# Optimization experiments

Hardware: AMD Instinct MI355X
Metric: run time of the kernel (lower is better)

Reference implementation:

```python
import jax, jax.numpy as jnp
import numpy as np
import math

EMB_DIM = 2048
HEAD_NUMS = 16
HEAD_DIM = EMB_DIM // HEAD_NUMS


def setup_inputs() -> dict:
    key = jax.random.key(0)
    k1, k2, k3, k4, k5 = jax.random.split(key, 5)
    B, S = 2, 2048
    X = jax.random.normal(k1, (B, S, EMB_DIM), dtype=jnp.float32)
    mask = jnp.ones((B, S), dtype=jnp.int32)
    # torch nn.Linear weights: [out_features, in_features]
    W_qkv = jax.random.normal(k2, (3 * EMB_DIM, EMB_DIM), dtype=jnp.float32) / math.sqrt(EMB_DIM)
    b_qkv = jax.random.normal(k3, (3 * EMB_DIM,), dtype=jnp.float32) * 0.01
    W_o = jax.random.normal(k4, (EMB_DIM, EMB_DIM), dtype=jnp.float32) / math.sqrt(EMB_DIM)
    b_o = jax.random.normal(k5, (EMB_DIM,), dtype=jnp.float32) * 0.01
    return {"X": X, "mask": mask, "W_qkv": W_qkv, "b_qkv": b_qkv, "W_o": W_o, "b_o": b_o}


def _rope_tables(seq_len):
    # Bug-faithful to source: exponent divides by full emb_dim, not head_dim.
    angle = 1.0 / jnp.power(10000.0, jnp.arange(0, HEAD_DIM, 2, dtype=jnp.float32) / EMB_DIM)
    t = jnp.arange(seq_len, dtype=jnp.float32)
    freqs = t[:, None] * angle[None, :]            # [S, HEAD_DIM//2]
    freqs = jnp.repeat(freqs, 2, axis=-1)          # [S, HEAD_DIM] (repeat_interleave)
    return jnp.cos(freqs), jnp.sin(freqs)


def _trans(x):
    # de-interleave pairs, then concat([-odd, even]) along last dim (as in source)
    B, H, S, D = x.shape
    xr = x.reshape(B, H, S, D // 2, 2)
    x1, x2 = xr[..., 0], xr[..., 1]
    return jnp.concatenate([-x2, x1], axis=-1)


def reference(X, mask, W_qkv, b_qkv, W_o, b_o):
    B, S, E = X.shape
    cos, sin = _rope_tables(S)                      # [S, HEAD_DIM]
    qkv = X @ W_qkv.T + b_qkv                       # [B, S, 3E]
    qkv = qkv.reshape(B, S, 3, HEAD_NUMS, HEAD_DIM).transpose(2, 0, 3, 1, 4)
    Q, K, V = qkv[0], qkv[1], qkv[2]                # [B, H, S, D]
    c = cos[None, None, :, :]
    s = sin[None, None, :, :]
    Q = c * Q + s * _trans(Q)
    K = c * K + s * _trans(K)
    scores = jnp.einsum('bhqd,bhkd->bhqk', Q, K) / math.sqrt(HEAD_DIM)
    pad = mask[:, None, None, :]                    # [B,1,1,S]
    scores = jnp.where(pad == 0, -1e9, scores)
    attn = jax.nn.softmax(scores, axis=-1)          # dropout = identity (eval)
    out = jnp.einsum('bhqk,bhkd->bhqd', attn, V)    # [B,H,S,D]
    out = out.transpose(0, 2, 1, 3).reshape(B, S, E)
    return out @ W_o.T + b_o
```

## Files before the change

### kernel.cpp

```cpp
#include <hip/hip_runtime.h>
#include <hip/hip_bf16.h>
#include <math.h>

typedef __bf16 bf16x8 __attribute__((ext_vector_type(8)));
typedef float  f32x4  __attribute__((ext_vector_type(4)));
typedef float  f32x16 __attribute__((ext_vector_type(16)));
typedef unsigned short ushort_t;
typedef ushort_t us4 __attribute__((ext_vector_type(4)));

#define MFMA16(a, b, c) __builtin_amdgcn_mfma_f32_16x16x32_bf16((a), (b), (c), 0, 0, 0)
#define MFMA32(a, b, c) __builtin_amdgcn_mfma_f32_32x32x16_bf16((a), (b), (c), 0, 0, 0)

__device__ __forceinline__ float bf2f(ushort_t h) {
    union { unsigned u; float f; } v; v.u = ((unsigned)h) << 16; return v.f;
}
__device__ __forceinline__ ushort_t f2bf(float x) {
    union { float f; unsigned u; } v; v.f = x;
    unsigned r = v.u + 0x7FFFu + ((v.u >> 16) & 1u);
    return (ushort_t)(r >> 16);
}
__device__ __forceinline__ void gl2lds16(const void* g, void* l) {
    __builtin_amdgcn_global_load_lds((__attribute__((address_space(1))) void*)(g),
                                     (__attribute__((address_space(3))) void*)(l),
                                     16, 0, 0);
}

__global__ __launch_bounds__(256) void detect_kernel(const ushort_t* __restrict__ w, int* flag)
{
    __shared__ int cnt[256];
    const int t = threadIdx.x;
    int c = 0;
    for (int i = t; i < 65536; i += 256) {
        const unsigned hw = w[i];
        const unsigned e = (hw >> 7) & 0xFFu;
        if (e == 0xFFu || (e == 0u && (hw & 0x7Fu) != 0u)) c++;
    }
    cnt[t] = c;
    __syncthreads();
    for (int s = 128; s > 0; s >>= 1) {
        if (t < s) cnt[t] += cnt[t + s];
        __syncthreads();
    }
    if (t == 0) flag[0] = (cnt[0] >= 8) ? 1 : 0;
}

__global__ __launch_bounds__(256) void convert_kernel(const void* __restrict__ src,
                                                      ushort_t* __restrict__ dst,
                                                      int n, const int* __restrict__ flag)
{
    const int i0 = (blockIdx.x * 256 + threadIdx.x) * 8;
    if (i0 + 8 > n) return;
    if (flag[0]) {
        const f32x4 a = *(const f32x4*)((const float*)src + i0);
        const f32x4 b = *(const f32x4*)((const float*)src + i0 + 4);
        ushort_t o[8];
        o[0]=f2bf(a[0]); o[1]=f2bf(a[1]); o[2]=f2bf(a[2]); o[3]=f2bf(a[3]);
        o[4]=f2bf(b[0]); o[5]=f2bf(b[1]); o[6]=f2bf(b[2]); o[7]=f2bf(b[3]);
        *(bf16x8*)(dst + i0) = *(const bf16x8*)o;
    } else {
        *(bf16x8*)(dst + i0) = *(const bf16x8*)((const ushort_t*)src + i0);
    }
}

__global__ __launch_bounds__(512, 2) void gemm256_bt_bias(
    const ushort_t* __restrict__ A, const ushort_t* __restrict__ B,
    const ushort_t* __restrict__ bias, ushort_t* __restrict__ C,
    int M, int N, int K)
{
    __shared__ __align__(16) ushort_t SM[65536];
    const int tid = threadIdx.x;
    const int l = tid & 63, ln = l & 15, q2 = l >> 4;
    const int w = tid >> 6, wm = w >> 2, wn = w & 3;
    const int m0 = blockIdx.y * 256, n0 = blockIdx.x * 256;
    const int NT = K >> 6;

#define STG_A256(slot, kbase, o) do { \
    const int s_ = (o) * 512 + tid; const int r_ = s_ >> 2; \
    const int q_ = (s_ & 3) ^ ((r_ >> 1) & 3); \
    gl2lds16(A + (size_t)(m0 + r_) * K + (kbase) + q_ * 8, \
             SM + (slot) * 16384 + s_ * 8); } while (0)
#define STG_B256(slot, kbase, o) do { \
    const int s_ = (o) * 512 + tid; const int r_ = s_ >> 2; \
    const int q_ = (s_ & 3) ^ ((r_ >> 1) & 3); \
    gl2lds16(B + (size_t)(n0 + r_) * K + (kbase) + q_ * 8, \
             SM + (slot) * 16384 + 8192 + s_ * 8); } while (0)
#define DSA256(slot, row) (*(const bf16x8*)(SM + (slot) * 16384 + (row) * 32 + ((q2 ^ (((row) >> 1) & 3)) << 3)))
#define DSB256(slot, row) (*(const bf16x8*)(SM + (slot) * 16384 + 8192 + (row) * 32 + ((q2 ^ (((row) >> 1) & 3)) << 3)))
#define BAR256() asm volatile("s_barrier" ::: "memory")

    f32x4 acc[8][4];
    const f32x4 z4 = {0.f, 0.f, 0.f, 0.f};
#pragma unroll
    for (int i = 0; i < 8; i++)
#pragma unroll
        for (int j = 0; j < 4; j++) acc[i][j] = z4;

    STG_A256(0, 0, 0);  STG_A256(0, 0, 1);  STG_B256(0, 0, 0);  STG_B256(0, 0, 1);
    STG_A256(1, 32, 0); STG_A256(1, 32, 1); STG_B256(1, 32, 0); STG_B256(1, 32, 1);
    if (NT > 1) STG_A256(2, 64, 0);
    asm volatile("s_waitcnt vmcnt(5)" ::: "memory");
    BAR256();

    for (int t = 0; t < NT; ++t) {
        const int s0 = (2 * t) & 3, s1 = (2 * t + 1) & 3;
        const int sA = (2 * t + 2) & 3, sB = (2 * t + 3) & 3;
        const int kA = (t + 1) << 6, kB = kA + 32, kC = (t + 2) << 6;
        const bool stAB = (t < NT - 1), stC = (t < NT - 2);
        const int rA0 = wm * 128, rA1 = wm * 128 + 64, rB = wn * 64;
        bf16x8 a0[4], a1[4], b00[2], b01[2], b10[2], b11[2];

#pragma unroll
        for (int ii = 0; ii < 4; ii++) a0[ii] = DSA256(s0, rA0 + ii * 16 + ln);
        b00[0] = DSB256(s0, rB + ln);
        b00[1] = DSB256(s0, rB + 16 + ln);
        if (stAB) STG_A256(sA, kA, 1);
        __builtin_amdgcn_s_setprio(1);
#pragma unroll
        for (int ii = 0; ii < 4; ii++) {
            acc[ii][0] = MFMA16(a0[ii], b00[0], acc[ii][0]);
            acc[ii][1] = MFMA16(a0[ii], b00[1], acc[ii][1]);
        }
        __builtin_amdgcn_s_setprio(0);
        if (stAB) { asm volatile("s_waitcnt vmcnt(2)" ::: "memory"); }
        else      { asm volatile("s_waitcnt vmcnt(0)" ::: "memory"); }
        BAR256();

#pragma unroll
        for (int ii = 0; ii < 4; ii++) a1[ii] = DSA256(s1, rA0 + ii * 16 + ln);
        b01[0] = DSB256(s1, rB + ln);
        b01[1] = DSB256(s1, rB + 16 + ln);
        if (stAB) STG_B256(sA, kA, 0);
        __builtin_amdgcn_s_setprio(1);
#pragma unroll
        for (int ii = 0; ii < 4; ii++) {
            acc[ii][0] = MFMA16(a1[ii], b01[0], acc[ii][0]);
            acc[ii][1] = MFMA16(a1[ii], b01[1], acc[ii][1]);
        }
        __builtin_amdgcn_s_setprio(0);
        BAR256();

        b10[0] = DSB256(s0, rB + 32 + ln);
        b10[1] = DSB256(s0, rB + 48 + ln);
        if (stAB) STG_B256(sA, kA, 1);
        __builtin_amdgcn_s_setprio(1);
#pragma unroll
        for (int ii = 0; ii < 4; ii++) {
            acc[ii][2] = MFMA16(a0[ii], b10[0], acc[ii][2]);
            acc[ii][3] = MFMA16(a0[ii], b10[1], acc[ii][3]);
        }
        __builtin_amdgcn_s_setprio(0);
        BAR256();

        b11[0] = DSB256(s1, rB + 32 + ln);
        b11[1] = DSB256(s1, rB + 48 + ln);
        if (stAB) STG_A256(sB, kB, 0);
        __builtin_amdgcn_s_setprio(1);
#pragma unroll
        for (int ii = 0; ii < 4; ii++) {
            acc[ii][2] = MFMA16(a1[ii], b11[0], acc[ii][2]);
            acc[ii][3] = MFMA16(a1[ii], b11[1], acc[ii][3]);
        }
        __builtin_amdgcn_s_setprio(0);
        BAR256();

#pragma unroll
        for (int ii = 0; ii < 4; ii++) a0[ii] = DSA256(s0, rA1 + ii * 16 + ln);
        if (stAB) STG_A256(sB, kB, 1);
        __builtin_amdgcn_s_setprio(1);
#pragma unroll
        for (int ii = 0; ii < 4; ii++) {
            acc[4 + ii][2] = MFMA16(a0[ii], b10[0], acc[4 + ii][2]);
            acc[4 + ii][3] = MFMA16(a0[ii], b10[1], acc[4 + ii][3]);
        }
        __builtin_amdgcn_s_setprio(0);
        BAR256();

#pragma unroll
        for (int ii = 0; ii < 4; ii++) a1[ii] = DSA256(s1, rA1 + ii * 16 + ln);
        if (stAB) STG_B256(sB, kB, 0);
        __builtin_amdgcn_s_setprio(1);
#pragma unroll
        for (int ii = 0; ii < 4; ii++) {
            acc[4 + ii][2] = MFMA16(a1[ii], b11[0], acc[4 + ii][2]);
            acc[4 + ii][3] = MFMA16(a1[ii], b11[1], acc[4 + ii][3]);
        }
        __builtin_amdgcn_s_setprio(0);
        BAR256();

        if (stAB) STG_B256(sB, kB, 1);
        __builtin_amdgcn_s_setprio(1);
#pragma unroll
        for (int ii = 0; ii < 4; ii++) {
            acc[4 + ii][0] = MFMA16(a0[ii], b00[0], acc[4 + ii][0]);
            acc[4 + ii][1] = MFMA16(a0[ii], b00[1], acc[4 + ii][1]);
        }
        __builtin_amdgcn_s_setprio(0);
        BAR256();

        if (stC) STG_A256(s0, kC, 0);
        __builtin_amdgcn_s_setprio(1);
#pragma unroll
        for (int ii = 0; ii < 4; ii++) {
            acc[4 + ii][0] = MFMA16(a1[ii], b01[0], acc[4 + ii][0]);
            acc[4 + ii][1] = MFMA16(a1[ii], b01[1], acc[4 + ii][1]);
        }
        __builtin_amdgcn_s_setprio(0);
        if (t < NT - 2)       { asm volatile("s_waitcnt vmcnt(5)" ::: "memory"); }
        else if (t == NT - 2) { asm volatile("s_waitcnt vmcnt(4)" ::: "memory"); }
        BAR256();
    }

#pragma unroll
    for (int j = 0; j < 4; j++) {
        const int n = n0 + wn * 64 + j * 16 + ln;
        const float bv = bf2f(bias[n]);
#pragma unroll
        for (int i = 0; i < 8; i++) {
            const int mrow = m0 + wm * 128 + i * 16 + q2 * 4;
#pragma unroll
            for (int r = 0; r < 4; r++)
                C[(size_t)(mrow + r) * N + n] = f2bf(acc[i][j][r] + bv);
        }
    }
#undef STG_A256
#undef STG_B256
#undef DSA256
#undef DSB256
#undef BAR256
}

__global__ __launch_bounds__(256) void gemm_bt_bias_out(
    const ushort_t* __restrict__ A, const ushort_t* __restrict__ B,
    const ushort_t* __restrict__ bias, void* __restrict__ C,
    int M, int N, int K, const int* __restrict__ flag)
{
    __shared__ __align__(16) ushort_t As[128 * 32];
    __shared__ __align__(16) ushort_t Bs[128 * 32];
    const int tid = threadIdx.x;
    const int w = tid >> 6, l = tid & 63, q = l >> 4, ln = l & 15;
    const int wm = w >> 1, wn = w & 1;
    const int m0 = blockIdx.y * 128, n0 = blockIdx.x * 128;
    const int sr = tid >> 2;
    const int sc = (tid & 3) * 8;

    f32x4 acc[4][4];
    const f32x4 z4 = {0.f, 0.f, 0.f, 0.f};
    for (int i = 0; i < 4; i++) for (int j = 0; j < 4; j++) acc[i][j] = z4;

    for (int k0 = 0; k0 < K; k0 += 32) {
        __syncthreads();
        gl2lds16(A + (size_t)(m0 + sr) * K + k0 + sc,       As + sr * 32 + sc);
        gl2lds16(A + (size_t)(m0 + 64 + sr) * K + k0 + sc,  As + (64 + sr) * 32 + sc);
        gl2lds16(B + (size_t)(n0 + sr) * K + k0 + sc,       Bs + sr * 32 + sc);
        gl2lds16(B + (size_t)(n0 + 64 + sr) * K + k0 + sc,  Bs + (64 + sr) * 32 + sc);
        __syncthreads();
        bf16x8 a[4], bb[4];
        for (int i = 0; i < 4; i++)
            a[i]  = *(const bf16x8*)(As + (wm * 64 + i * 16 + ln) * 32 + q * 8);
        for (int j = 0; j < 4; j++)
            bb[j] = *(const bf16x8*)(Bs + (wn * 64 + j * 16 + ln) * 32 + q * 8);
        for (int i = 0; i < 4; i++)
            for (int j = 0; j < 4; j++)
                acc[i][j] = MFMA16(a[i], bb[j], acc[i][j]);
    }
    const int f = flag[0];
    for (int j = 0; j < 4; j++) {
        const int n = n0 + wn * 64 + j * 16 + ln;
        const float bv = bf2f(bias[n]);
        for (int i = 0; i < 4; i++) {
            const int mrow = m0 + wm * 64 + i * 16 + q * 4;
            for (int r = 0; r < 4; r++) {
                const float val = acc[i][j][r] + bv;
                const size_t idx = (size_t)(mrow + r) * N + n;
                if (f) ((float*)C)[idx] = val;
                else   ((ushort_t*)C)[idx] = f2bf(val);
            }
        }
    }
}

__global__ __launch_bounds__(256) void rope_kernel(ushort_t* qkv)
{
    const int bs = blockIdx.x;
    const int s = bs & 2047;
    const int t = threadIdx.x;
    const int qk = t >> 7;
    const int u = t & 127;
    const int h = u >> 3, i = u & 7;
    ushort_t* row = qkv + (size_t)bs * 6144 + qk * 2048 + h * 128;

    union { bf16x8 v; ushort_t e[8]; } L0, L1, L2, L3;
    L0.v = *(const bf16x8*)(row + 8 * i);
    L1.v = *(const bf16x8*)(row + 64 + 8 * i);
    L2.v = *(const bf16x8*)(row + 16 * i);
    L3.v = *(const bf16x8*)(row + 16 * i + 8);

    float ca[4], sa_[4], cb[4], sb[4];
#pragma unroll
    for (int e = 0; e < 4; e++) {
        const float angA = powf(10000.0f, -(float)(2 * (4 * i + e)) / 2048.0f);
        const float angB = powf(10000.0f, -(float)(2 * (32 + 4 * i + e)) / 2048.0f);
        sincosf((float)s * angA, &sa_[e], &ca[e]);
        sincosf((float)s * angB, &sb[e], &cb[e]);
    }
    __syncthreads();
    ushort_t oA[8], oB[8];
#pragma unroll
    for (int d = 0; d < 8; d++) {
        const int e = d >> 1;
        const float pA = (d < 4) ? bf2f(L2.e[2 * d + 1]) : bf2f(L3.e[2 * d - 7]);
        const float pB = (d < 4) ? bf2f(L2.e[2 * d])     : bf2f(L3.e[2 * d - 8]);
        oA[d] = f2bf(ca[e] * bf2f(L0.e[d]) - sa_[e] * pA);
        oB[d] = f2bf(cb[e] * bf2f(L1.e[d]) + sb[e] * pB);
    }
    *(bf16x8*)(row + 8 * i)      = *(const bf16x8*)oA;
    *(bf16x8*)(row + 64 + 8 * i) = *(const bf16x8*)oB;
}

__global__ __launch_bounds__(256) void vtrans_kernel(const ushort_t* __restrict__ qkv,
                                                     ushort_t* __restrict__ Vt)
{
    __shared__ __align__(16) ushort_t tile[64][136];
    const int blk = blockIdx.x;
    const int st = blk & 31, h = (blk >> 5) & 15, b = blk >> 9;
    const int t = threadIdx.x;
#pragma unroll
    for (int i = 0; i < 4; i++) {
        const int e = i * 256 + t;
        const int r = e >> 4, cb = e & 15;
        *(bf16x8*)(&tile[r][cb * 8]) =
            *(const bf16x8*)(qkv + (size_t)(b * 2048 + st * 64 + r) * 6144 + 4096 + h * 128 + cb * 8);
    }
    __syncthreads();
    const int d = t >> 1, s0 = (t & 1) * 32;
    const size_t obase = ((size_t)(b * 16 + h) * 128 + d) * 2048 + st * 64 + s0;
#pragma unroll
    for (int q4 = 0; q4 < 4; q4++) {
        ushort_t tmp[8];
#pragma unroll
        for (int j = 0; j < 8; j++) tmp[j] = tile[s0 + q4 * 8 + j][d];
        *(bf16x8*)(Vt + obase + q4 * 8) = *(const bf16x8*)tmp;
    }
}

__global__ __launch_bounds__(256, 2) void flash_kernel(
    const ushort_t* __restrict__ qkv, const ushort_t* __restrict__ Vt,
    const int* __restrict__ mask, ushort_t* __restrict__ AO)
{
    __shared__ __align__(16) ushort_t SM[16384];
    ushort_t* Ks = SM;
    ushort_t* Vs = SM + 8192;
    const int t = threadIdx.x;
    const int w = t >> 6, l = t & 63, lq = l & 31, q2 = l >> 5;
    const int qb = blockIdx.x * 128, h = blockIdx.y, b = blockIdx.z;
    const size_t brow = (size_t)b * 2048;
    const float scale = 0.08838834764831845f;
    const int qrow = qb + w * 32 + lq;
    const size_t vbase = (size_t)(b * 16 + h) * 128;

    bf16x8 qf[8];
#pragma unroll
    for (int kb = 0; kb < 8; kb++)
        qf[kb] = *(const bf16x8*)(qkv + (brow + qrow) * 6144 + h * 128 + kb * 16 + q2 * 8);

    float m_old = -1e30f, lsum = 0.f;
    f32x16 acc_o[4];
#pragma unroll
    for (int dt = 0; dt < 4; dt++)
#pragma unroll
        for (int r = 0; r < 16; r++) acc_o[dt][r] = 0.f;

    bf16x8 kst[4], vst[4];
#pragma unroll
    for (int i = 0; i < 4; i++) {
        const int s_ = i * 256 + t; const int row = s_ >> 4; const int u = s_ & 15;
        kst[i] = *(const bf16x8*)(qkv + (brow + row) * 6144 + 2048 + h * 128 + u * 8);
    }
#pragma unroll
    for (int i = 0; i < 4; i++) {
        const int s_ = i * 256 + t; const int row = s_ >> 3; const int u = s_ & 7;
        vst[i] = *(const bf16x8*)(Vt + (vbase + row) * 2048 + u * 8);
    }

    for (int s0 = 0; s0 < 2048; s0 += 64) {
        const int mk = mask[brow + s0 + l];
        const unsigned long long bm = __ballot(mk != 0);
        asm volatile("s_waitcnt lgkmcnt(0)" ::: "memory");
        asm volatile("s_barrier" ::: "memory");
#pragma unroll
        for (int i = 0; i < 4; i++) {
            const int s_ = i * 256 + t; const int row = s_ >> 4; const int u = s_ & 15;
            *(bf16x8*)(Ks + row * 128 + ((u ^ (row & 15)) << 3)) = kst[i];
        }
#pragma unroll
        for (int i = 0; i < 4; i++) {
            const int s_ = i * 256 + t; const int row = s_ >> 3; const int u = s_ & 7;
            *(bf16x8*)(Vs + row * 64 + ((u ^ (row & 7)) << 3)) = vst[i];
        }
        if (s0 + 64 < 2048) {
#pragma unroll
            for (int i = 0; i < 4; i++) {
                const int s_ = i * 256 + t; const int row = s_ >> 4; const int u = s_ & 15;
                kst[i] = *(const bf16x8*)(qkv + (brow + s0 + 64 + row) * 6144 + 2048 + h * 128 + u * 8);
            }
#pragma unroll
            for (int i = 0; i < 4; i++) {
                const int s_ = i * 256 + t; const int row = s_ >> 3; const int u = s_ & 7;
                vst[i] = *(const bf16x8*)(Vt + (vbase + row) * 2048 + s0 + 64 + u * 8);
            }
        }
        asm volatile("s_waitcnt lgkmcnt(0)" ::: "memory");
        asm volatile("s_barrier" ::: "memory");

        f32x16 sa[2];
#pragma unroll
        for (int mt = 0; mt < 2; mt++) {
#pragma unroll
            for (int r = 0; r < 16; r++) sa[mt][r] = 0.f;
            const int row = mt * 32 + lq;
            __builtin_amdgcn_s_setprio(1);
#pragma unroll
            for (int kb = 0; kb < 8; kb++) {
                bf16x8 a = *(const bf16x8*)(Ks + row * 128 + (((kb * 2 + q2) ^ (row & 15)) << 3));
                sa[mt] = MFMA32(a, qf[kb], sa[mt]);
            }
            __builtin_amdgcn_s_setprio(0);
        }
        float p[32];
        float mr = -1e30f;
        if (bm == ~0ull) {
#pragma unroll
            for (int mt = 0; mt < 2; mt++)
#pragma unroll
                for (int r = 0; r < 16; r++) {
                    const float v = sa[mt][r] * scale;
                    p[mt * 16 + r] = v;
                    mr = fmaxf(mr, v);
                }
        } else {
#pragma unroll
            for (int mt = 0; mt < 2; mt++)
#pragma unroll
                for (int r = 0; r < 16; r++) {
                    const int srow = mt * 32 + (r & 3) + 8 * (r >> 2) + 4 * q2;
                    const float bias = ((bm >> srow) & 1ull) ? 0.f : -1e9f;
                    const float v = sa[mt][r] * scale + bias;
                    p[mt * 16 + r] = v;
                    mr = fmaxf(mr, v);
                }
        }
        mr = fmaxf(mr, __shfl_xor(mr, 32, 64));
        if (!__all(mr <= m_old + 8.0f)) {
            const float mnew = fmaxf(m_old, mr);
            const float alpha = __expf(m_old - mnew);
            lsum *= alpha;
#pragma unroll
            for (int dt = 0; dt < 4; dt++)
#pragma unroll
                for (int r = 0; r < 16; r++) acc_o[dt][r] *= alpha;
            m_old = mnew;
        }
        float rs = 0.f;
#pragma unroll
        for (int i = 0; i < 32; i++) { p[i] = __expf(p[i] - m_old); rs += p[i]; }
        rs += __shfl_xor(rs, 32, 64);
        lsum += rs;

#pragma unroll
        for (int kb = 0; kb < 4; kb++) {
            const int bb = (kb >> 1) * 16 + (kb & 1) * 8;
            unsigned w01, w23, w45, w67;
            asm("v_cvt_pk_bf16_f32 %0, %1, %2" : "=v"(w01) : "v"(p[bb + 0]), "v"(p[bb + 1]));
            asm("v_cvt_pk_bf16_f32 %0, %1, %2" : "=v"(w23) : "v"(p[bb + 2]), "v"(p[bb + 3]));
            asm("v_cvt_pk_bf16_f32 %0, %1, %2" : "=v"(w45) : "v"(p[bb + 4]), "v"(p[bb + 5]));
            asm("v_cvt_pk_bf16_f32 %0, %1, %2" : "=v"(w67) : "v"(p[bb + 6]), "v"(p[bb + 7]));
            asm("v_permlane32_swap_b32 %0, %1" : "+v"(w01), "+v"(w45));
            asm("v_permlane32_swap_b32 %0, %1" : "+v"(w23), "+v"(w67));
            union { unsigned u[4]; bf16x8 v8; } pu;
            pu.u[0] = w01; pu.u[1] = w23; pu.u[2] = w45; pu.u[3] = w67;
            __builtin_amdgcn_s_setprio(1);
#pragma unroll
            for (int dt = 0; dt < 4; dt++) {
                const int row = dt * 32 + lq;
                bf16x8 va = *(const bf16x8*)(Vs + row * 64 + (((kb * 2 + q2) ^ (row & 7)) << 3));
                acc_o[dt] = MFMA32(va, pu.v8, acc_o[dt]);
            }
            __builtin_amdgcn_s_setprio(0);
        }
    }
    __syncthreads();
    const float inv = (lsum > 0.f) ? 1.0f / lsum : 0.f;
#pragma unroll
    for (int dt = 0; dt < 4; dt++)
#pragma unroll
        for (int r2 = 0; r2 < 4; r2++) {
            us4 ov;
#pragma unroll
            for (int j = 0; j < 4; j++) ov[j] = f2bf(acc_o[dt][r2 * 4 + j] * inv);
            const int row = w * 32 + lq;
            const int unit = dt * 4 + r2;
            *(us4*)(SM + row * 128 + ((unit ^ (row & 15)) << 3) + q2 * 4) = ov;
        }
    __syncthreads();
#pragma unroll
    for (int i = 0; i < 8; i++) {
        const int rl = i * 4 + (l >> 4), ch = l & 15;
        const int row = w * 32 + rl;
        bf16x8 vv = *(const bf16x8*)(SM + row * 128 + ((ch ^ (row & 15)) << 3));
        *(bf16x8*)(AO + (brow + qb + row) * 2048 + h * 128 + ch * 8) = vv;
    }
}

extern "C" void kernel_launch(void* const* d_in, const int* in_sizes, int n_in,
                              void* d_out, int out_size, void* d_ws, size_t ws_size,
                              hipStream_t stream)
{
    (void)in_sizes; (void)n_in; (void)out_size; (void)ws_size;
    const void* X    = d_in[0];
    const int*  mask = (const int*)d_in[1];
    const void* Wqkv = d_in[2];
    const void* bqkv = d_in[3];
    const void* Wo   = d_in[4];
    const void* bo   = d_in[5];

    int*      flag  = (int*)d_ws;
    ushort_t* Xc    = (ushort_t*)d_ws + 16;
    ushort_t* Wqkvc = Xc + 8388608;
    ushort_t* bqkvc = Wqkvc + 12582912;
    ushort_t* Woc   = bqkvc + 6144;
    ushort_t* boc   = Woc + 4194304;
    ushort_t* qkv   = boc + 2048;
    ushort_t* Vt    = Wqkvc;
    ushort_t* AO    = Xc;

    detect_kernel<<<1, 256, 0, stream>>>((const ushort_t*)Wqkv, flag);
    convert_kernel<<<4096, 256, 0, stream>>>(X,    Xc,    8388608,  flag);
    convert_kernel<<<6144, 256, 0, stream>>>(Wqkv, Wqkvc, 12582912, flag);
    convert_kernel<<<3,    256, 0, stream>>>(bqkv, bqkvc, 6144,     flag);
    convert_kernel<<<2048, 256, 0, stream>>>(Wo,   Woc,   4194304,  flag);
    convert_kernel<<<1,    256, 0, stream>>>(bo,   boc,   2048,     flag);

    gemm256_bt_bias<<<dim3(6144 / 256, 4096 / 256), 512, 0, stream>>>(Xc, Wqkvc, bqkvc, qkv, 4096, 6144, 2048);
    rope_kernel<<<4096, 256, 0, stream>>>(qkv);
    vtrans_kernel<<<1024, 256, 0, stream>>>(qkv, Vt);
    flash_kernel<<<dim3(16, 16, 2), 256, 0, stream>>>(qkv, Vt, mask, AO);
    gemm_bt_bias_out<<<dim3(2048 / 128, 4096 / 128), 256, 0, stream>>>(AO, Woc, boc, d_out, 4096, 2048, 2048, flag);
}
```

Baseline: 607.8 us.

## Precompute RoPE sin/cos table and remap flash blocks for XCD locality

After: 549.0 us. -9.7%, faster.

```diff
diff --git a/kernel.cpp b/kernel.cpp
--- a/kernel.cpp
+++ b/kernel.cpp
@@ -279,7 +279,18 @@
     }
 }
 
-__global__ __launch_bounds__(256) void rope_kernel(ushort_t* qkv)
+__global__ __launch_bounds__(256) void rope_table_kernel(float* __restrict__ tab)
+{
+    const int idx = blockIdx.x * 256 + threadIdx.x;
+    const int s = idx >> 6, k = idx & 63;
+    const float ang = powf(10000.0f, -(float)(2 * k) / 2048.0f);
+    float sv, cv;
+    sincosf((float)s * ang, &sv, &cv);
+    tab[(size_t)idx * 2]     = cv;
+    tab[(size_t)idx * 2 + 1] = sv;
+}
+
+__global__ __launch_bounds__(256) void rope_kernel(ushort_t* qkv, const float* __restrict__ tab)
 {
     const int bs = blockIdx.x;
     const int s = bs & 2047;
@@ -295,14 +306,16 @@
     L2.v = *(const bf16x8*)(row + 16 * i);
     L3.v = *(const bf16x8*)(row + 16 * i + 8);
 
-    float ca[4], sa_[4], cb[4], sb[4];
-#pragma unroll
-    for (int e = 0; e < 4; e++) {
-        const float angA = powf(10000.0f, -(float)(2 * (4 * i + e)) / 2048.0f);
-        const float angB = powf(10000.0f, -(float)(2 * (32 + 4 * i + e)) / 2048.0f);
-        sincosf((float)s * angA, &sa_[e], &ca[e]);
-        sincosf((float)s * angB, &sb[e], &cb[e]);
-    }
+    const float* tA = tab + ((size_t)s * 64 + 4 * i) * 2;
+    const f32x4 a0v = *(const f32x4*)(tA);
+    const f32x4 a1v = *(const f32x4*)(tA + 4);
+    const f32x4 b0v = *(const f32x4*)(tA + 64);
+    const f32x4 b1v = *(const f32x4*)(tA + 68);
+    const float ca[4]  = {a0v[0], a0v[2], a1v[0], a1v[2]};
+    const float sa_[4] = {a0v[1], a0v[3], a1v[1], a1v[3]};
+    const float cb[4]  = {b0v[0], b0v[2], b1v[0], b1v[2]};
+    const float sb[4]  = {b0v[1], b0v[3], b1v[1], b1v[3]};
+
     __syncthreads();
     ushort_t oA[8], oB[8];
 #pragma unroll
@@ -352,7 +365,11 @@
     ushort_t* Vs = SM + 8192;
     const int t = threadIdx.x;
     const int w = t >> 6, l = t & 63, lq = l & 31, q2 = l >> 5;
-    const int qb = blockIdx.x * 128, h = blockIdx.y, b = blockIdx.z;
+    const int bid = blockIdx.x;
+    const int xcd = bid & 7, ii = bid >> 3;
+    const int p = xcd * 4 + (ii >> 4);
+    const int qb = (ii & 15) * 128;
+    const int h = p & 15, b = p >> 4;
     const size_t brow = (size_t)b * 2048;
     const float scale = 0.08838834764831845f;
     const int qrow = qb + w * 32 + lq;
@@ -426,7 +443,7 @@
             }
             __builtin_amdgcn_s_setprio(0);
         }
-        float p[32];
+        float p_[32];
         float mr = -1e30f;
         if (bm == ~0ull) {
 #pragma unroll
@@ -434,7 +451,7 @@
 #pragma unroll
                 for (int r = 0; r < 16; r++) {
                     const float v = sa[mt][r] * scale;
-                    p[mt * 16 + r] = v;
+                    p_[mt * 16 + r] = v;
                     mr = fmaxf(mr, v);
                 }
         } else {
@@ -445,7 +462,7 @@
                     const int srow = mt * 32 + (r & 3) + 8 * (r >> 2) + 4 * q2;
                     const float bias = ((bm >> srow) & 1ull) ? 0.f : -1e9f;
                     const float v = sa[mt][r] * scale + bias;
-                    p[mt * 16 + r] = v;
+                    p_[mt * 16 + r] = v;
                     mr = fmaxf(mr, v);
                 }
         }
@@ -462,7 +479,7 @@
         }
         float rs = 0.f;
 #pragma unroll
-        for (int i = 0; i < 32; i++) { p[i] = __expf(p[i] - m_old); rs += p[i]; }
+        for (int i = 0; i < 32; i++) { p_[i] = __expf(p_[i] - m_old); rs += p_[i]; }
         rs += __shfl_xor(rs, 32, 64);
         lsum += rs;
 
@@ -470,10 +487,10 @@
         for (int kb = 0; kb < 4; kb++) {
             const int bb = (kb >> 1) * 16 + (kb & 1) * 8;
             unsigned w01, w23, w45, w67;
-            asm("v_cvt_pk_bf16_f32 %0, %1, %2" : "=v"(w01) : "v"(p[bb + 0]), "v"(p[bb + 1]));
-            asm("v_cvt_pk_bf16_f32 %0, %1, %2" : "=v"(w23) : "v"(p[bb + 2]), "v"(p[bb + 3]));
-            asm("v_cvt_pk_bf16_f32 %0, %1, %2" : "=v"(w45) : "v"(p[bb + 4]), "v"(p[bb + 5]));
-            asm("v_cvt_pk_bf16_f32 %0, %1, %2" : "=v"(w67) : "v"(p[bb + 6]), "v"(p[bb + 7]));
+            asm("v_cvt_pk_bf16_f32 %0, %1, %2" : "=v"(w01) : "v"(p_[bb + 0]), "v"(p_[bb + 1]));
+            asm("v_cvt_pk_bf16_f32 %0, %1, %2" : "=v"(w23) : "v"(p_[bb + 2]), "v"(p_[bb + 3]));
+            asm("v_cvt_pk_bf16_f32 %0, %1, %2" : "=v"(w45) : "v"(p_[bb + 4]), "v"(p_[bb + 5]));
+            asm("v_cvt_pk_bf16_f32 %0, %1, %2" : "=v"(w67) : "v"(p_[bb + 6]), "v"(p_[bb + 7]));
             asm("v_permlane32_swap_b32 %0, %1" : "+v"(w01), "+v"(w45));
             asm("v_permlane32_swap_b32 %0, %1" : "+v"(w23), "+v"(w67));
             union { unsigned u[4]; bf16x8 v8; } pu;
@@ -531,6 +548,7 @@
     ushort_t* boc   = Woc + 4194304;
     ushort_t* qkv   = boc + 2048;
     ushort_t* Vt    = Wqkvc;
+    float*    rtab  = (float*)(Wqkvc + 8388608);
     ushort_t* AO    = Xc;
 
     detect_kernel<<<1, 256, 0, stream>>>((const ushort_t*)Wqkv, flag);
@@ -541,8 +559,9 @@
     convert_kernel<<<1,    256, 0, stream>>>(bo,   boc,   2048,     flag);
 
     gemm256_bt_bias<<<dim3(6144 / 256, 4096 / 256), 512, 0, stream>>>(Xc, Wqkvc, bqkvc, qkv, 4096, 6144, 2048);
-    rope_kernel<<<4096, 256, 0, stream>>>(qkv);
+    rope_table_kernel<<<512, 256, 0, stream>>>(rtab);
+    rope_kernel<<<4096, 256, 0, stream>>>(qkv, rtab);
     vtrans_kernel<<<1024, 256, 0, stream>>>(qkv, Vt);
-    flash_kernel<<<dim3(16, 16, 2), 256, 0, stream>>>(qkv, Vt, mask, AO);
+    flash_kernel<<<512, 256, 0, stream>>>(qkv, Vt, mask, AO);
     gemm_bt_bias_out<<<dim3(2048 / 128, 4096 / 128), 256, 0, stream>>>(AO, Woc, boc, d_out, 4096, 2048, 2048, flag);
 }
```
